# Kernel optimization log

Hardware: AMD Instinct MI355X
Metric: run time of the kernel (lower is better)

## Reference

```python
import jax, jax.numpy as jnp
import numpy as np

LN_EPS = 1e-5

def _next_fast_len(n):
    # smallest 5-smooth integer >= n (matches scipy.fftpack.next_fast_len)
    while True:
        m = n
        for p in (2, 3, 5):
            while m % p == 0:
                m //= p
        if m == 1:
            return n
        n += 1

def _conv1d_fft(x, w):
    # x: (b, h, N, d), convolved along axis -2 against w: (h, M) along axis -1.
    # Matches the torch reference: multiply by conj(rfft(w)), roll by -1, take last N.
    N = x.shape[-2]
    M = w.shape[-1]
    L = _next_fast_len(N + M - 1)
    fx = jnp.fft.rfft(x, n=L, axis=-2)                    # (b, h, F, d) complex
    fw = jnp.fft.rfft(w, n=L, axis=-1)                    # (h, F) complex
    out = jnp.fft.irfft(fx * jnp.conj(fw)[..., None], L, axis=-2)
    out = jnp.roll(out, -1, axis=-2)
    return out[..., L - N:, :]                            # (b, h, N, d)

def setup_inputs() -> dict:
    key = jax.random.key(0)
    ks = jax.random.split(key, 5)
    b, n, d, h = 4, 4096, 1024, 8
    dh = d // h
    s = 0.02
    return {
        "x": jax.random.normal(ks[0], (b, n, d), jnp.float32),
        "ln_gamma": jnp.ones((d,), jnp.float32),
        "ln_beta": jnp.zeros((d,), jnp.float32),
        "w_in": jax.random.normal(ks[1], (d, d), jnp.float32) * s,
        "b_in": jnp.zeros((d,), jnp.float32),
        "initial_state": jax.random.normal(ks[2], (h, dh), jnp.float32),
        "alpha": jax.random.normal(ks[3], (h,), jnp.float32),
        "w_out": jax.random.normal(ks[4], (d, d), jnp.float32) * s,
        "b_out": jnp.zeros((d,), jnp.float32),
    }

def reference(x, ln_gamma, ln_beta, w_in, b_in, initial_state, alpha, w_out, b_out):
    b, n, d = x.shape
    h, dh = initial_state.shape
    # LayerNorm
    mu = jnp.mean(x, axis=-1, keepdims=True)
    var = jnp.mean((x - mu) ** 2, axis=-1, keepdims=True)
    xn = (x - mu) * jax.lax.rsqrt(var + LN_EPS) * ln_gamma + ln_beta
    # project_in (torch Linear: y = x @ W.T + b)
    xp = xn @ w_in.T + b_in
    # b n (h d) -> b h n d
    xh = xp.reshape(b, n, h, dh).transpose(0, 2, 1, 3)
    # prepend learned initial state, then first difference along n
    init = jnp.broadcast_to(initial_state[None, :, None, :], (b, h, 1, dh))
    xc = jnp.concatenate([init, xh], axis=2)
    xd = xc[:, :, 1:] - xc[:, :, :-1]                     # (b, h, n, dh)
    # EMA weights per head
    a = jax.nn.sigmoid(alpha)[:, None]                    # (h, 1)
    ar = jnp.arange(n)
    w = a * (1.0 - a) ** ar[::-1]                         # (h, n)
    out = _conv1d_fft(xd, w)
    # initial-state contribution
    init_w = (1.0 - a) ** (ar + 1)                        # (h, n)
    out = out + init_w[:, :, None] * initial_state[:, None, :]
    # b h n d -> b n (h d), then project_out
    out = out.transpose(0, 2, 1, 3).reshape(b, n, d)
    return out @ w_out.T + b_out
```

## Files before the change

### kernel.cpp

```cpp
#include <hip/hip_runtime.h>
#include <stdint.h>

typedef float  f32x4 __attribute__((ext_vector_type(4)));
typedef __bf16 bf16x8 __attribute__((ext_vector_type(8)));
typedef short  s16x8 __attribute__((ext_vector_type(8)));
typedef unsigned short u16;

static __device__ __forceinline__ u16 f2bf(float f) {
  unsigned u = __float_as_uint(f);
  u += 0x7fffu + ((u >> 16) & 1u);
  return (u16)(u >> 16);
}
static __device__ __forceinline__ float bf2f(u16 u) {
  return __uint_as_float(((unsigned)u) << 16);
}

static __device__ __forceinline__ void async_copy16(void* lds, const void* g) {
  __builtin_amdgcn_global_load_lds(
      (const __attribute__((address_space(1))) unsigned int*)g,
      (__attribute__((address_space(3))) unsigned int*)lds, 16, 0, 0);
}

__global__ __launch_bounds__(256) void ln_cvt_k(const float* __restrict__ x,
                                                const float* __restrict__ g,
                                                const float* __restrict__ b,
                                                u16* __restrict__ xn,
                                                const float* __restrict__ w0,
                                                const float* __restrict__ w1,
                                                u16* __restrict__ o0,
                                                u16* __restrict__ o1) {
  const int D = 1024, Mrows = 16384, n4 = 262144;
  const int tid = threadIdx.x;
  if (blockIdx.x >= Mrows) {
    int i = (blockIdx.x - Mrows) * 256 + tid;
    const float* in = (i < n4) ? w0 : w1;
    u16* out = (i < n4) ? o0 : o1;
    int idx = (i < n4) ? i : i - n4;
    float4 v = reinterpret_cast<const float4*>(in)[idx];
    ushort4 o;
    o.x = f2bf(v.x); o.y = f2bf(v.y); o.z = f2bf(v.z); o.w = f2bf(v.w);
    reinterpret_cast<ushort4*>(out)[idx] = o;
    return;
  }
  const int row = blockIdx.x;
  const float4 v = reinterpret_cast<const float4*>(x + (size_t)row * D)[tid];
  float s  = v.x + v.y + v.z + v.w;
  float s2 = v.x * v.x + v.y * v.y + v.z * v.z + v.w * v.w;
  #pragma unroll
  for (int off = 32; off > 0; off >>= 1) {
    s  += __shfl_down(s, off);
    s2 += __shfl_down(s2, off);
  }
  __shared__ float red[8];
  const int lane = tid & 63, wv = tid >> 6;
  if (lane == 0) { red[wv] = s; red[4 + wv] = s2; }
  __syncthreads();
  s  = red[0] + red[1] + red[2] + red[3];
  s2 = red[4] + red[5] + red[6] + red[7];
  const float mu   = s * (1.0f / D);
  const float var  = s2 * (1.0f / D) - mu * mu;
  const float rstd = rsqrtf(var + 1e-5f);
  const float4 gv = reinterpret_cast<const float4*>(g)[tid];
  const float4 bv = reinterpret_cast<const float4*>(b)[tid];
  ushort4 o;
  o.x = f2bf((v.x - mu) * rstd * gv.x + bv.x);
  o.y = f2bf((v.y - mu) * rstd * gv.y + bv.y);
  o.z = f2bf((v.z - mu) * rstd * gv.z + bv.z);
  o.w = f2bf((v.w - mu) * rstd * gv.w + bv.w);
  reinterpret_cast<ushort4*>(xn + (size_t)row * D)[tid] = o;
}

template<int MODE>
__global__ __launch_bounds__(512, 2) void gemm_bt_k(const u16* __restrict__ A,
                                                    const u16* __restrict__ Bm,
                                                    const float* __restrict__ bias,
                                                    void* __restrict__ Cv,
                                                    const float* __restrict__ alpha,
                                                    float* __restrict__ Lp,
                                                    int M, int N, int K) {
  const int tid  = threadIdx.x;
  const int lane = tid & 63;
  const int wv   = tid >> 6;
  const int wrr  = wv >> 2;
  const int wcc  = wv & 3;
  const int ntN  = N >> 8;
  const int nwg  = (M >> 8) * ntN;
  const int bid  = blockIdx.x;
  const int wgid = (bid & 7) * (nwg >> 3) + (bid >> 3);
  const int mt = wgid / ntN, nt = wgid % ntN;
  const int m0 = mt << 8, n0 = nt << 8;

  __shared__ __align__(16) u16 smem[65536];
  __shared__ float sRed[256];

  const int u   = tid >> 3;
  const int tch = tid & 7;
  const int csw = (tch ^ (u & 7)) << 3;
  const int lofs = u * 64 + (tch << 3);
  const u16* gA = A  + (size_t)(m0 + u) * K + csw;
  const u16* gB = Bm + (size_t)(n0 + u) * K + csw;

  f32x4 acc[8][4];
  #pragma unroll
  for (int i = 0; i < 8; ++i)
    #pragma unroll
    for (int j = 0; j < 4; ++j) acc[i][j] = f32x4{0.f, 0.f, 0.f, 0.f};

  const int fr  = lane & 15;
  const int fkc = lane >> 4;
  const int sx  = fr & 7;
  const int nk  = K >> 6;
  int buf = 0;

  #pragma unroll
  for (int r = 0; r < 4; ++r) {
    async_copy16(&smem[lofs + r * 4096], gA + (size_t)(r * 64) * K);
    async_copy16(&smem[32768 + lofs + r * 4096], gB + (size_t)(r * 64) * K);
  }
  __syncthreads();

  for (int t = 0; t < nk; ++t) {
    if (t + 1 < nk) {
      const size_t ko = (size_t)(t + 1) << 6;
      const int nb = (buf ^ 1) * 16384;
      #pragma unroll
      for (int r = 0; r < 4; ++r) {
        async_copy16(&smem[nb + lofs + r * 4096], gA + ko + (size_t)(r * 64) * K);
        async_copy16(&smem[32768 + nb + lofs + r * 4096], gB + ko + (size_t)(r * 64) * K);
      }
    }
    const u16* bA = smem + buf * 16384;
    const u16* bB = smem + 32768 + buf * 16384;
    #pragma unroll
    for (int s = 0; s < 2; ++s) {
      const int ch = ((((s << 2) + fkc) ^ sx) << 3);
      s16x8 af[8], bfr[4];
      #pragma unroll
      for (int i = 0; i < 8; ++i)
        af[i] = *reinterpret_cast<const s16x8*>(
            &bA[(wrr * 128 + i * 16 + fr) * 64 + ch]);
      #pragma unroll
      for (int j = 0; j < 4; ++j)
        bfr[j] = *reinterpret_cast<const s16x8*>(
            &bB[(wcc * 64 + j * 16 + fr) * 64 + ch]);
      #pragma unroll
      for (int i = 0; i < 8; ++i)
        #pragma unroll
        for (int j = 0; j < 4; ++j)
          acc[i][j] = __builtin_amdgcn_mfma_f32_16x16x32_bf16(
              __builtin_bit_cast(bf16x8, af[i]),
              __builtin_bit_cast(bf16x8, bfr[j]), acc[i][j], 0, 0, 0);
    }
    __syncthreads();
    buf ^= 1;
  }

  float* sC = (float*)smem;
  const int cr = (lane >> 4) << 2;
  const int cc = lane & 15;
  float bv[4];
  #pragma unroll
  for (int nj = 0; nj < 4; ++nj) bv[nj] = bias[n0 + wcc * 64 + nj * 16 + cc];

  #pragma unroll
  for (int p = 0; p < 2; ++p) {
    __syncthreads();
    if (wrr == p) {
      #pragma unroll
      for (int mi = 0; mi < 8; ++mi)
        #pragma unroll
        for (int nj = 0; nj < 4; ++nj)
          #pragma unroll
          for (int rr = 0; rr < 4; ++rr) {
            const int row = mi * 16 + cr + rr;
            const int col = wcc * 64 + nj * 16 + cc;
            sC[row * 256 + (col ^ ((row & 4) << 2))] = acc[mi][nj][rr] + bv[nj];
          }
    }
    __syncthreads();
    #pragma unroll 4
    for (int it = 0; it < 16; ++it) {
      const int row  = it * 8 + (tid >> 6);
      const int col0 = (tid & 63) * 4;
      f32x4 v = *(const f32x4*)&sC[row * 256 + (col0 ^ ((row & 4) << 2))];
      const size_t goff = (size_t)(m0 + p * 128 + row) * N + n0 + col0;
      if (MODE == 1) {
        ushort4 o; o.x = f2bf(v[0]); o.y = f2bf(v[1]); o.z = f2bf(v[2]); o.w = f2bf(v[3]);
        *(ushort4*)&((u16*)Cv)[goff] = o;
      } else {
        *(f32x4*)&((float*)Cv)[goff] = v;
      }
    }
    if (MODE == 1) {
      const int col = tid & 255;
      const int hh = (n0 + col) >> 7;
      const float a  = 1.0f / (1.0f + __expf(-alpha[hh]));
      const float rw = 1.0f - a;
      float r64 = rw;
      #pragma unroll
      for (int s = 0; s < 6; ++s) r64 *= r64;
      const bool lo = (tid < 256);
      const int rbase  = lo ? 1 : 64;
      const int nsteps = lo ? 63 : 64;
      float prev = sC[(rbase - 1) * 256 + (col ^ (((rbase - 1) & 4) << 2))];
      float L = 0.f;
      #pragma unroll 8
      for (int t = rbase; t < rbase + 64; ++t) {
        if (t - rbase >= nsteps) break;
        const float w = sC[t * 256 + (col ^ ((t & 4) << 2))];
        L = rw * L + a * (w - prev);
        prev = w;
      }
      if (!lo) sRed[col] = L;
      __syncthreads();
      if (lo) {
        const float Lt = r64 * L + sRed[col];
        const int bb = m0 >> 12;
        const int q  = ((m0 >> 7) & 31) + p;
        Lp[((size_t)bb * 32 + q) * 1024 + n0 + col] = Lt;
      }
    }
  }
}

__global__ __launch_bounds__(256) void ema_carry_k(const u16* __restrict__ xpb,
                                                   const float* __restrict__ alpha,
                                                   const float* __restrict__ init,
                                                   float* __restrict__ carry) {
  const int Dd = 1024, nCh = 32;
  const int idx = blockIdx.x * 256 + threadIdx.x;
  const int c  = idx & (Dd - 1);
  const int bb = idx >> 10;
  const int h = c >> 7;
  const float a = 1.0f / (1.0f + __expf(-alpha[h]));
  const float r = 1.0f - a;
  float q_ = r, r127 = 1.0f;
  #pragma unroll
  for (int s = 0; s < 7; ++s) { r127 *= q_; q_ *= q_; }
  const float rT = r127 * r;
  float L[32], v0[32], vm[32];
  #pragma unroll
  for (int q = 0; q < nCh; ++q) {
    const size_t rowb = (size_t)bb * 4096 + (size_t)q * 128;
    L[q]  = carry[((size_t)bb * nCh + q) * Dd + c];
    v0[q] = bf2f(xpb[rowb * Dd + c]);
    vm[q] = bf2f(xpb[(rowb + 127) * Dd + c]);
  }
  float cin = init[c];
  float prevv = cin;
  #pragma unroll
  for (int q = 0; q < nCh; ++q) {
    const float Lf = L[q] + a * r127 * (v0[q] - prevv);
    carry[((size_t)bb * nCh + q) * Dd + c] = cin;
    cin = rT * cin + Lf;
    prevv = vm[q];
  }
}

__global__ __launch_bounds__(256) void ema_apply_k(const u16* __restrict__ xp,
                                                   const float* __restrict__ alpha,
                                                   const float* __restrict__ init,
                                                   const float* __restrict__ carry,
                                                   u16* __restrict__ ob) {
  const int Nn = 4096, Dd = 1024, T = 128, nCh = 32;
  int bid = blockIdx.x;
  const int cg = bid & 3;  bid >>= 2;
  const int q  = bid & 31; bid >>= 5;
  const int bb = bid;
  const int c = cg * 256 + threadIdx.x;
  const int h = c >> 7;
  const float a = 1.0f / (1.0f + __expf(-alpha[h]));
  const float r = 1.0f - a;
  const u16* px = xp + ((size_t)bb * Nn + (size_t)q * T) * Dd + c;
  u16* po = ob + ((size_t)bb * Nn + (size_t)q * T) * Dd + c;
  float O = carry[((size_t)bb * nCh + q) * Dd + c];
  float p0 = (q == 0) ? init[c] : bf2f(px[-Dd]);
  #pragma unroll 4
  for (int t = 0; t < T; ++t) {
    const float v = bf2f(px[(size_t)t * Dd]);
    O = r * O + a * (v - p0);
    p0 = v;
    po[(size_t)t * Dd] = f2bf(O);
  }
}

extern "C" void kernel_launch(void* const* d_in, const int* in_sizes, int n_in,
                              void* d_out, int out_size, void* d_ws, size_t ws_size,
                              hipStream_t stream) {
  const float* x     = (const float*)d_in[0];
  const float* ln_g  = (const float*)d_in[1];
  const float* ln_b  = (const float*)d_in[2];
  const float* w_in  = (const float*)d_in[3];
  const float* b_in  = (const float*)d_in[4];
  const float* init  = (const float*)d_in[5];
  const float* alpha = (const float*)d_in[6];
  const float* w_out = (const float*)d_in[7];
  const float* b_out = (const float*)d_in[8];
  float* out = (float*)d_out;

  const int B = 4, N = 4096, D = 1024;
  const int M = B * N;

  char* p = (char*)d_ws;
  u16*   xn  = (u16*)p; p += (size_t)M * D * sizeof(u16);
  u16*   wi  = (u16*)p; p += (size_t)D * D * sizeof(u16);
  u16*   wo  = (u16*)p; p += (size_t)D * D * sizeof(u16);
  u16*   xpb = (u16*)p; p += (size_t)M * D * sizeof(u16);
  float* cr  = (float*)p; p += (size_t)B * 32 * D * sizeof(float);
  u16*   ob  = (u16*)p;

  ln_cvt_k<<<dim3(M + 2048), dim3(256), 0, stream>>>(
      x, ln_g, ln_b, xn, w_in, w_out, wi, wo);
  gemm_bt_k<1><<<dim3((M / 256) * (D / 256)), dim3(512), 0, stream>>>(
      xn, wi, b_in, xpb, alpha, cr, M, D, D);
  ema_carry_k<<<dim3(B * D / 256), dim3(256), 0, stream>>>(xpb, alpha, init, cr);
  ema_apply_k<<<dim3(B * 32 * 4), dim3(256), 0, stream>>>(xpb, alpha, init, cr, ob);
  gemm_bt_k<0><<<dim3((M / 256) * (D / 256)), dim3(512), 0, stream>>>(
      ob, wo, b_out, out, nullptr, nullptr, M, D, D);
}
```

Before: 137.5 us.

## Restructure GEMM main loop into quadrant-staged pipeline with interleaved async loads

Rewrites the bf16 GEMM inner loop to split each 64-wide K step into four sub-tile phases (A/B halves). Each phase reads fragments from LDS, issues part of the next tile's global-to-LDS async copies, then runs MFMAs at raised wave priority between barriers. Global rows for A and B are permuted so that each quadrant's loads land in a dedicated LDS region, keeping the accumulator layout compatible with the existing epilogue. The aim is to overlap memory traffic with MFMA work at finer granularity and cut register pressure from fragment loads. The cost is many more barriers per K step and explicit vmcnt waits that must track outstanding copies exactly.

Measured after the change: 138.9 us. No clear change (+1.1%).

```diff
diff --git a/kernel.cpp b/kernel.cpp
--- a/kernel.cpp
+++ b/kernel.cpp
@@ -70,6 +70,47 @@
   reinterpret_cast<ushort4*>(xn + (size_t)row * D)[tid] = o;
 }
 
+static __device__ __forceinline__ s16x8 ldfrag(const u16* b, int row, int ks,
+                                               int fkc, int sx) {
+  return *reinterpret_cast<const s16x8*>(
+      &b[row * 64 + ((((ks << 2) + fkc) ^ sx) << 3)]);
+}
+template<int MH>
+static __device__ __forceinline__ void rdA(const u16* bA, s16x8 (&af)[4][2],
+                                           int wrr, int fr, int fkc, int sx) {
+  #pragma unroll
+  for (int i = 0; i < 4; ++i)
+    #pragma unroll
+    for (int ks = 0; ks < 2; ++ks)
+      af[i][ks] = ldfrag(bA, MH * 128 + wrr * 64 + i * 16 + fr, ks, fkc, sx);
+}
+template<int NH>
+static __device__ __forceinline__ void rdB(const u16* bB, s16x8 (&bfr)[2][2],
+                                           int wcc, int fr, int fkc, int sx) {
+  #pragma unroll
+  for (int j = 0; j < 2; ++j)
+    #pragma unroll
+    for (int ks = 0; ks < 2; ++ks)
+      bfr[j][ks] = ldfrag(bB, NH * 128 + wcc * 32 + j * 16 + fr, ks, fkc, sx);
+}
+template<int MH, int NH>
+static __device__ __forceinline__ void mmq(f32x4 (&acc)[8][4],
+                                           const s16x8 (&af)[4][2],
+                                           const s16x8 (&bfr)[2][2]) {
+  __builtin_amdgcn_s_setprio(1);
+  #pragma unroll
+  for (int i = 0; i < 4; ++i)
+    #pragma unroll
+    for (int j = 0; j < 2; ++j)
+      #pragma unroll
+      for (int ks = 0; ks < 2; ++ks)
+        acc[MH * 4 + i][NH * 2 + j] = __builtin_amdgcn_mfma_f32_16x16x32_bf16(
+            __builtin_bit_cast(bf16x8, af[i][ks]),
+            __builtin_bit_cast(bf16x8, bfr[j][ks]), acc[MH * 4 + i][NH * 2 + j],
+            0, 0, 0);
+  __builtin_amdgcn_s_setprio(0);
+}
+
 template<int MODE>
 __global__ __launch_bounds__(512, 2) void gemm_bt_k(const u16* __restrict__ A,
                                                     const u16* __restrict__ Bm,
@@ -97,8 +138,16 @@
   const int tch = tid & 7;
   const int csw = (tch ^ (u & 7)) << 3;
   const int lofs = u * 64 + (tch << 3);
-  const u16* gA = A  + (size_t)(m0 + u) * K + csw;
-  const u16* gB = Bm + (size_t)(n0 + u) * K + csw;
+  constexpr int amap[4] = {0, 2, 1, 3};
+  const u16* gAr[4];
+  const u16* gBr[4];
+  #pragma unroll
+  for (int r = 0; r < 4; ++r) {
+    gAr[r] = A + (size_t)(m0 + amap[r] * 64 + u) * K + csw;
+    const int l = r * 64 + u;
+    const int grow = ((l >> 5) & 3) * 64 + (l >> 7) * 32 + (l & 31);
+    gBr[r] = Bm + (size_t)(n0 + grow) * K + csw;
+  }
 
   f32x4 acc[8][4];
   #pragma unroll
@@ -110,50 +159,75 @@
   const int fkc = lane >> 4;
   const int sx  = fr & 7;
   const int nk  = K >> 6;
-  int buf = 0;
-
-  #pragma unroll
-  for (int r = 0; r < 4; ++r) {
-    async_copy16(&smem[lofs + r * 4096], gA + (size_t)(r * 64) * K);
-    async_copy16(&smem[32768 + lofs + r * 4096], gB + (size_t)(r * 64) * K);
-  }
-  __syncthreads();
-
-  for (int t = 0; t < nk; ++t) {
-    if (t + 1 < nk) {
-      const size_t ko = (size_t)(t + 1) << 6;
-      const int nb = (buf ^ 1) * 16384;
-      #pragma unroll
-      for (int r = 0; r < 4; ++r) {
-        async_copy16(&smem[nb + lofs + r * 4096], gA + ko + (size_t)(r * 64) * K);
-        async_copy16(&smem[32768 + nb + lofs + r * 4096], gB + ko + (size_t)(r * 64) * K);
-      }
-    }
-    const u16* bA = smem + buf * 16384;
-    const u16* bB = smem + 32768 + buf * 16384;
-    #pragma unroll
-    for (int s = 0; s < 2; ++s) {
-      const int ch = ((((s << 2) + fkc) ^ sx) << 3);
-      s16x8 af[8], bfr[4];
-      #pragma unroll
-      for (int i = 0; i < 8; ++i)
-        af[i] = *reinterpret_cast<const s16x8*>(
-            &bA[(wrr * 128 + i * 16 + fr) * 64 + ch]);
-      #pragma unroll
-      for (int j = 0; j < 4; ++j)
-        bfr[j] = *reinterpret_cast<const s16x8*>(
-            &bB[(wcc * 64 + j * 16 + fr) * 64 + ch]);
-      #pragma unroll
-      for (int i = 0; i < 8; ++i)
-        #pragma unroll
-        for (int j = 0; j < 4; ++j)
-          acc[i][j] = __builtin_amdgcn_mfma_f32_16x16x32_bf16(
-              __builtin_bit_cast(bf16x8, af[i]),
-              __builtin_bit_cast(bf16x8, bfr[j]), acc[i][j], 0, 0, 0);
-    }
-    __syncthreads();
-    buf ^= 1;
-  }
+  const int nit = nk >> 1;
+
+#define ST2(base, p0, p1, ko) \
+  async_copy16(&smem[(base) + lofs], (p0) + (ko)); \
+  async_copy16(&smem[(base) + 4096 + lofs], (p1) + (ko));
+#define BAR __builtin_amdgcn_s_barrier()
+
+  ST2(0,     gAr[0], gAr[1], 0)
+  ST2(32768, gBr[0], gBr[1], 0)
+  ST2(8192,  gAr[2], gAr[3], 0)
+  ST2(40960, gBr[2], gBr[3], 0)
+  ST2(49152, gBr[0], gBr[1], 64)
+  ST2(24576, gAr[2], gAr[3], 64)
+  asm volatile("s_waitcnt vmcnt(4)" ::: "memory");
+  BAR;
+
+  const u16* bA0 = smem;
+  const u16* bB0 = smem + 32768;
+  const u16* bA1 = smem + 16384;
+  const u16* bB1 = smem + 49152;
+  s16x8 af[4][2], bfr[2][2];
+
+  for (int it = 0; it < nit; ++it) {
+    const size_t ko1 = (size_t)(2 * it + 1) << 6;
+    const size_t ko2 = (size_t)(2 * it + 2) << 6;
+    const size_t ko3 = (size_t)(2 * it + 3) << 6;
+    const bool pf = (it + 1 < nit);
+
+    rdA<0>(bA0, af, wrr, fr, fkc, sx);
+    rdB<0>(bB0, bfr, wcc, fr, fkc, sx);
+    ST2(16384, gAr[0], gAr[1], ko1)
+    BAR; mmq<0, 0>(acc, af, bfr); BAR;
+
+    rdA<1>(bA0, af, wrr, fr, fkc, sx);
+    ST2(57344, gBr[2], gBr[3], ko1)
+    BAR; mmq<1, 0>(acc, af, bfr); BAR;
+
+    rdB<1>(bB0, bfr, wcc, fr, fkc, sx);
+    if (pf) { ST2(32768, gBr[0], gBr[1], ko2) }
+    BAR; mmq<1, 1>(acc, af, bfr); BAR;
+
+    rdA<0>(bA0, af, wrr, fr, fkc, sx);
+    if (pf) { ST2(8192, gAr[2], gAr[3], ko2) }
+    BAR; mmq<0, 1>(acc, af, bfr);
+    if (pf) { asm volatile("s_waitcnt vmcnt(4)" ::: "memory"); }
+    else    { asm volatile("s_waitcnt vmcnt(0)" ::: "memory"); }
+    BAR;
+
+    rdA<0>(bA1, af, wrr, fr, fkc, sx);
+    rdB<0>(bB1, bfr, wcc, fr, fkc, sx);
+    if (pf) { ST2(0, gAr[0], gAr[1], ko2) }
+    BAR; mmq<0, 0>(acc, af, bfr); BAR;
+
+    rdA<1>(bA1, af, wrr, fr, fkc, sx);
+    if (pf) { ST2(40960, gBr[2], gBr[3], ko2) }
+    BAR; mmq<1, 0>(acc, af, bfr); BAR;
+
+    rdB<1>(bB1, bfr, wcc, fr, fkc, sx);
+    if (pf) { ST2(49152, gBr[0], gBr[1], ko3) }
+    BAR; mmq<1, 1>(acc, af, bfr); BAR;
+
+    rdA<0>(bA1, af, wrr, fr, fkc, sx);
+    if (pf) { ST2(24576, gAr[2], gAr[3], ko3) }
+    BAR; mmq<0, 1>(acc, af, bfr);
+    if (pf) { asm volatile("s_waitcnt vmcnt(4)" ::: "memory"); }
+    BAR;
+  }
+#undef ST2
+#undef BAR
 
   float* sC = (float*)smem;
   const int cr = (lane >> 4) << 2;
```
